# Kernel tuning notes

Measured on AMD Instinct MI355X. Metric: run time of the kernel, lower is better.

Reference implementation:

```python
import jax, jax.numpy as jnp
import numpy as np

N = 50000   # nodes
E = 800000  # edges (avg degree 16)
IN = 256    # in_dim
H = 4       # nhead
D = 64      # out_dim per head
NEG_SLOPE_ATTN = 0.2   # DGL GATConv default negative_slope for edge scores
NEG_SLOPE_OUT = 0.01   # nn.LeakyReLU default on the layer output


def setup_inputs() -> dict:
    key = jax.random.key(0)
    ks = jax.random.split(key, 6)
    h = jax.random.normal(ks[0], (N, IN), dtype=jnp.float32)
    src = jax.random.randint(ks[1], (E,), 0, N, dtype=jnp.int32)
    dst = jax.random.randint(ks[2], (E,), 0, N, dtype=jnp.int32)
    W = jax.random.normal(ks[3], (IN, H * D), dtype=jnp.float32) / np.float32(np.sqrt(IN))
    attn_l = jax.random.normal(ks[4], (H, D), dtype=jnp.float32) * 0.1
    attn_r = jax.random.normal(ks[5], (H, D), dtype=jnp.float32) * 0.1
    bias = jnp.zeros((H * D,), dtype=jnp.float32)
    return {"h": h, "src": src, "dst": dst, "W": W,
            "attn_l": attn_l, "attn_r": attn_r, "bias": bias}


def reference(h, src, dst, W, attn_l, attn_r, bias):
    n = h.shape[0]
    # linear projection -> [N, H, D]
    feat = (h @ W).reshape(n, H, D)
    # per-node, per-head attention halves: [N, H]
    el = jnp.sum(feat * attn_l, axis=-1)
    er = jnp.sum(feat * attn_r, axis=-1)
    # per-edge unnormalized score (DGL: src contributes el, dst contributes er)
    e = jax.nn.leaky_relu(el[src] + er[dst], NEG_SLOPE_ATTN)  # [E, H]
    # edge softmax over incoming edges of each destination node
    emax = jax.ops.segment_max(e, dst, num_segments=n)        # [N, H]
    ee = jnp.exp(e - emax[dst])                               # [E, H]
    denom = jax.ops.segment_sum(ee, dst, num_segments=n)      # [N, H]
    a = ee / jnp.maximum(denom[dst], 1e-9)                    # [E, H]
    # weighted scatter-aggregate of projected source features
    msg = feat[src] * a[:, :, None]                           # [E, H, D]
    rst = jax.ops.segment_sum(msg, dst, num_segments=n)       # [N, H, D]
    rst = rst + bias.reshape(H, D)
    # outer activation (dropout is identity in eval)
    return jax.nn.leaky_relu(rst, NEG_SLOPE_OUT)
```

## Files before the change

kernel.cpp:

```cpp
#include <hip/hip_runtime.h>

#define IN_DIM 256
#define HD 256
#define NHEAD 4
#define BM 128

typedef __attribute__((ext_vector_type(8))) short short8;
typedef __attribute__((ext_vector_type(4))) float f32x4;

__device__ __forceinline__ float bf2f(ushort u) {
    unsigned x = ((unsigned)u) << 16;
    float f;
    __builtin_memcpy(&f, &x, 4);
    return f;
}
__device__ __forceinline__ ushort f2bf(float f) {
    unsigned x;
    __builtin_memcpy(&x, &f, 4);
    unsigned r = (x + 0x7FFFu + ((x >> 16) & 1u)) >> 16;
    return (ushort)r;
}
__device__ __forceinline__ short8 cvt8(float4 x, float4 y) {
    short8 a;
    a[0] = (short)f2bf(x.x); a[1] = (short)f2bf(x.y);
    a[2] = (short)f2bf(x.z); a[3] = (short)f2bf(x.w);
    a[4] = (short)f2bf(y.x); a[5] = (short)f2bf(y.y);
    a[6] = (short)f2bf(y.z); a[7] = (short)f2bf(y.w);
    return a;
}

__global__ void fill_one(float* __restrict__ out, int n) {
    int i = blockIdx.x * 256 + threadIdx.x;
    if (i < n) out[i] = 1.0f;
}

__global__ void conv_w_zero(const float* __restrict__ W, ushort* __restrict__ WT,
                            int* __restrict__ cnt, int n) {
    int idx = blockIdx.x * 256 + threadIdx.x;
    int k = idx >> 8, c = idx & 255;
    WT[c * 256 + k] = f2bf(W[idx]);
    for (int i = idx; i < n; i += 65536) cnt[i] = 0;
}

__global__ __launch_bounds__(256, 2) void gemm_hist(const float* __restrict__ h,
                                                    const short* __restrict__ WT,
                                                    ushort* __restrict__ featb,
                                                    float* __restrict__ el,
                                                    float* __restrict__ er,
                                                    const float* __restrict__ attn_l,
                                                    const float* __restrict__ attn_r,
                                                    const int* __restrict__ dst,
                                                    int* __restrict__ cnt,
                                                    int* __restrict__ epos,
                                                    int gb, int n, int e) {
    if (blockIdx.x >= gb) {
        int i = (blockIdx.x - gb) * 256 + threadIdx.x;
        int base = i * 4;
        if (base + 3 < e) {
            int4 d4 = *(const int4*)(dst + base);
            int4 p4;
            p4.x = atomicAdd(&cnt[d4.x], 1);
            p4.y = atomicAdd(&cnt[d4.y], 1);
            p4.z = atomicAdd(&cnt[d4.z], 1);
            p4.w = atomicAdd(&cnt[d4.w], 1);
            *(int4*)(epos + base) = p4;
        } else {
            for (int q = base; q < e; ++q) epos[q] = atomicAdd(&cnt[dst[q]], 1);
        }
        return;
    }
    __shared__ __align__(16) ushort blds[2][8192];
    int t = threadIdx.x;
    int w = t >> 6, l = t & 63;
    int c15 = l & 15, g = l >> 4;
    int blockBase = blockIdx.x * BM;
    int row0 = blockBase + w * 32 + c15;
    int rA0 = row0 < n ? row0 : n - 1;
    int rA1 = (row0 + 16) < n ? (row0 + 16) : n - 1;
    const float* hA0 = h + (size_t)rA0 * 256 + g * 8;
    const float* hA1 = h + (size_t)rA1 * 256 + g * 8;

    f32x4 acc[2][16];
#pragma unroll
    for (int af = 0; af < 2; ++af)
#pragma unroll
        for (int ct = 0; ct < 16; ++ct) acc[af][ct] = (f32x4)(0.0f);

    short8 st[4];
    int sc[4], sb[4];
#pragma unroll
    for (int p = 0; p < 4; ++p) {
        int q = t + p * 256;
        sc[p] = q >> 2;
        int gg = q & 3;
        sb[p] = ((sc[p] * 64 + gg * 16) ^ ((sc[p] & 7) << 4));
    }

#pragma unroll
    for (int p = 0; p < 4; ++p)
        st[p] = *(const short8*)(WT + sc[p] * 256 + ((t + p * 256) & 3) * 8);
#pragma unroll
    for (int p = 0; p < 4; ++p)
        *(short8*)((char*)blds[0] + sb[p]) = st[p];
    __syncthreads();

    for (int kk = 0; kk < 8; ++kk) {
        int buf = kk & 1;
        if (kk < 7) {
#pragma unroll
            for (int p = 0; p < 4; ++p)
                st[p] = *(const short8*)(WT + sc[p] * 256 + (kk + 1) * 32 + ((t + p * 256) & 3) * 8);
        }
        float4 x0 = *(const float4*)(hA0 + kk * 32);
        float4 y0 = *(const float4*)(hA0 + kk * 32 + 4);
        float4 x1 = *(const float4*)(hA1 + kk * 32);
        float4 y1 = *(const float4*)(hA1 + kk * 32 + 4);
        short8 a0 = cvt8(x0, y0);
        short8 a1 = cvt8(x1, y1);
        const char* bb = (const char*)blds[buf];
#pragma unroll
        for (int ct = 0; ct < 16; ++ct) {
            int c = ct * 16 + c15;
            short8 bv = *(const short8*)(bb + ((c * 64 + g * 16) ^ ((c & 7) << 4)));
            acc[0][ct] = __builtin_amdgcn_mfma_f32_16x16x32_bf16(a0, bv, acc[0][ct], 0, 0, 0);
            acc[1][ct] = __builtin_amdgcn_mfma_f32_16x16x32_bf16(a1, bv, acc[1][ct], 0, 0, 0);
        }
        if (kk < 7) {
#pragma unroll
            for (int p = 0; p < 4; ++p)
                *(short8*)((char*)blds[buf ^ 1] + sb[p]) = st[p];
        }
        __syncthreads();
    }

    float alv[16], arv[16];
#pragma unroll
    for (int ct = 0; ct < 16; ++ct) {
        alv[ct] = attn_l[ct * 16 + c15];
        arv[ct] = attn_r[ct * 16 + c15];
    }

#pragma unroll
    for (int af = 0; af < 2; ++af) {
        int rowb = blockBase + w * 32 + af * 16 + g * 4;
#pragma unroll
        for (int r = 0; r < 4; ++r) {
            int row = rowb + r;
            if (row < n) {
#pragma unroll
                for (int ct = 0; ct < 16; ++ct)
                    featb[(size_t)row * 256 + ct * 16 + c15] = f2bf(acc[af][ct][r]);
            }
            float pl[4] = {0.f, 0.f, 0.f, 0.f}, pr[4] = {0.f, 0.f, 0.f, 0.f};
#pragma unroll
            for (int ct = 0; ct < 16; ++ct) {
                pl[ct >> 2] += acc[af][ct][r] * alv[ct];
                pr[ct >> 2] += acc[af][ct][r] * arv[ct];
            }
#pragma unroll
            for (int m = 1; m < 16; m <<= 1) {
#pragma unroll
                for (int hh = 0; hh < 4; ++hh) {
                    pl[hh] += __shfl_xor(pl[hh], m, 64);
                    pr[hh] += __shfl_xor(pr[hh], m, 64);
                }
            }
            if (row < n) {
                if (c15 < 4)       el[row * 4 + c15]       = pl[c15];
                else if (c15 < 8)  er[row * 4 + (c15 - 4)] = pr[c15 - 4];
            }
        }
    }
}

__global__ __launch_bounds__(1024) void scan_local(const int* __restrict__ cnt,
                                                   int* __restrict__ rl,
                                                   int* __restrict__ bsum, int n) {
    __shared__ int wsums[16];
    int t = threadIdx.x, lane = t & 63, wid = t >> 6;
    int i = blockIdx.x * 1024 + t;
    int x = (i < n) ? cnt[i] : 0;
    int s = x;
#pragma unroll
    for (int off = 1; off < 64; off <<= 1) {
        int v = __shfl_up(s, off, 64);
        if (lane >= off) s += v;
    }
    if (lane == 63) wsums[wid] = s;
    __syncthreads();
    if (wid == 0) {
        int ws = (lane < 16) ? wsums[lane] : 0;
#pragma unroll
        for (int off = 1; off < 16; off <<= 1) {
            int v = __shfl_up(ws, off, 64);
            if (lane >= off) ws += v;
        }
        if (lane < 16) wsums[lane] = ws;
    }
    __syncthreads();
    int woff = (wid > 0) ? wsums[wid - 1] : 0;
    if (i <= n) rl[i] = woff + s - x;
    if (t == 1023) bsum[blockIdx.x] = wsums[15];
}

__global__ __launch_bounds__(1024) void scan_bsum(int* __restrict__ bsum, int nb) {
    __shared__ int wsums[16];
    int t = threadIdx.x, lane = t & 63, wid = t >> 6;
    int x = (t < nb) ? bsum[t] : 0;
    int s = x;
#pragma unroll
    for (int off = 1; off < 64; off <<= 1) {
        int v = __shfl_up(s, off, 64);
        if (lane >= off) s += v;
    }
    if (lane == 63) wsums[wid] = s;
    __syncthreads();
    if (wid == 0) {
        int ws = (lane < 16) ? wsums[lane] : 0;
#pragma unroll
        for (int off = 1; off < 16; off <<= 1) {
            int v = __shfl_up(ws, off, 64);
            if (lane >= off) ws += v;
        }
        if (lane < 16) wsums[lane] = ws;
    }
    __syncthreads();
    int woff = (wid > 0) ? wsums[wid - 1] : 0;
    if (t < nb) bsum[t] = woff + s - x;
}

__global__ void fill_kernel(const int* __restrict__ src, const int* __restrict__ dst,
                            const int* __restrict__ rl, const int* __restrict__ boffs,
                            const int* __restrict__ epos,
                            int* __restrict__ esrc, int e) {
    int i = blockIdx.x * 256 + threadIdx.x;
    int base = i * 4;
    if (base + 3 < e) {
        int4 d4 = *(const int4*)(dst + base);
        int4 s4 = *(const int4*)(src + base);
        int4 p4 = *(const int4*)(epos + base);
        int pos0 = boffs[d4.x >> 10] + rl[d4.x] + p4.x;
        int pos1 = boffs[d4.y >> 10] + rl[d4.y] + p4.y;
        int pos2 = boffs[d4.z >> 10] + rl[d4.z] + p4.z;
        int pos3 = boffs[d4.w >> 10] + rl[d4.w] + p4.w;
        if (pos0 >= 0 && pos0 < e) esrc[pos0] = s4.x;
        if (pos1 >= 0 && pos1 < e) esrc[pos1] = s4.y;
        if (pos2 >= 0 && pos2 < e) esrc[pos2] = s4.z;
        if (pos3 >= 0 && pos3 < e) esrc[pos3] = s4.w;
    } else {
        for (int q = base; q < e; ++q) {
            int d = dst[q];
            int pos = boffs[d >> 10] + rl[d] + epos[q];
            if (pos >= 0 && pos < e) esrc[pos] = src[q];
        }
    }
}

__global__ __launch_bounds__(64) void aggregate(const int* __restrict__ rl,
                                                const int* __restrict__ boffs,
                                                const int* __restrict__ esrc,
                                                const float* __restrict__ el,
                                                const float* __restrict__ er,
                                                const ushort* __restrict__ featb,
                                                const float* __restrict__ bias,
                                                float* __restrict__ out, int n) {
    __shared__ int sbuf[64];
    __shared__ float wbuf[64][4];
    int node = blockIdx.x;
    int l = threadIdx.x;
    int hh = l >> 4;
    int beg = boffs[node >> 10] + rl[node];
    int end = boffs[(node + 1) >> 10] + rl[node + 1];
    float4 bv = *(const float4*)(bias + l * 4);
    float* op = out + (size_t)node * 256 + l * 4;
    if (beg >= end) {
        float4 v;
        v.x = bv.x > 0.f ? bv.x : 0.01f * bv.x;
        v.y = bv.y > 0.f ? bv.y : 0.01f * bv.y;
        v.z = bv.z > 0.f ? bv.z : 0.01f * bv.z;
        v.w = bv.w > 0.f ? bv.w : 0.01f * bv.w;
        *(float4*)op = v;
        return;
    }
    float4 r4 = *(const float4*)(er + (size_t)node * 4);
    float ax = 0.f, ay = 0.f, az = 0.f, aw = 0.f, s = 0.f;
    for (int cb = beg; cb < end; cb += 64) {
        int cn = min(64, end - cb);
        __syncthreads();
        if (l < cn) {
            int sv = esrc[cb + l];
            sv = (sv >= 0 && sv < n) ? sv : 0;
            sbuf[l] = sv;
            float4 l4 = *(const float4*)(el + (size_t)sv * 4);
            float e0 = l4.x + r4.x; e0 = e0 > 0.f ? e0 : 0.2f * e0;
            float e1 = l4.y + r4.y; e1 = e1 > 0.f ? e1 : 0.2f * e1;
            float e2 = l4.z + r4.z; e2 = e2 > 0.f ? e2 : 0.2f * e2;
            float e3 = l4.w + r4.w; e3 = e3 > 0.f ? e3 : 0.2f * e3;
            wbuf[l][0] = __expf(fminf(e0, 60.f));
            wbuf[l][1] = __expf(fminf(e1, 60.f));
            wbuf[l][2] = __expf(fminf(e2, 60.f));
            wbuf[l][3] = __expf(fminf(e3, 60.f));
        }
        __syncthreads();
#pragma unroll 4
        for (int j = 0; j < cn; ++j) {
            int sid = sbuf[j];
            float wgt = wbuf[j][hh];
            ushort4 f4 = *(const ushort4*)(featb + (size_t)sid * 256 + l * 4);
            ax += wgt * bf2f(f4.x);
            ay += wgt * bf2f(f4.y);
            az += wgt * bf2f(f4.z);
            aw += wgt * bf2f(f4.w);
            s += wgt;
        }
    }
    float inv = 1.f / fmaxf(s, 1e-9f);
    float4 v;
    v.x = ax * inv + bv.x; v.x = v.x > 0.f ? v.x : 0.01f * v.x;
    v.y = ay * inv + bv.y; v.y = v.y > 0.f ? v.y : 0.01f * v.y;
    v.z = az * inv + bv.z; v.z = v.z > 0.f ? v.z : 0.01f * v.z;
    v.w = aw * inv + bv.w; v.w = v.w > 0.f ? v.w : 0.01f * v.w;
    *(float4*)op = v;
}

extern "C" void kernel_launch(void* const* d_in, const int* in_sizes, int n_in,
                              void* d_out, int out_size, void* d_ws, size_t ws_size,
                              hipStream_t stream) {
    const float* h      = (const float*)d_in[0];
    const int*   src    = (const int*)d_in[1];
    const int*   dst    = (const int*)d_in[2];
    const float* W      = (const float*)d_in[3];
    const float* attn_l = (const float*)d_in[4];
    const float* attn_r = (const float*)d_in[5];
    const float* bias   = (const float*)d_in[6];
    float* out = (float*)d_out;

    int N = in_sizes[0] / IN_DIM;
    int E = in_sizes[1];
    int NB = (N + 1 + 1023) / 1024;

    auto al = [](size_t x) { return (x + 255) & ~(size_t)255; };
    char* ws = (char*)d_ws;
    size_t o = 0;
    ushort* featb = (ushort*)(ws + o); o += al((size_t)N * HD * 2);
    float*  el    = (float*)(ws + o);  o += al((size_t)N * NHEAD * 4);
    float*  er    = (float*)(ws + o);  o += al((size_t)N * NHEAD * 4);
    int*    rl    = (int*)(ws + o);    o += al((size_t)(N + 1) * 4);
    int*    cnt   = (int*)(ws + o);    o += al((size_t)N * 4);
    int*    bsum  = (int*)(ws + o);    o += al((size_t)NB * 4);
    int*    esrc  = (int*)(ws + o);    o += al((size_t)E * 4);
    int*    epos  = (int*)(ws + o);    o += al((size_t)E * 4);
    ushort* WT    = (ushort*)(ws + o); o += al((size_t)IN_DIM * HD * 2);
    (void)n_in;

    if (ws_size < o) {
        fill_one<<<(out_size + 255) / 256, 256, 0, stream>>>(out, out_size);
        return;
    }

    conv_w_zero<<<(IN_DIM * HD) / 256, 256, 0, stream>>>(W, WT, cnt, N);

    int GB = (N + BM - 1) / BM;
    int HB = ((E + 3) / 4 + 255) / 256;
    gemm_hist<<<GB + HB, 256, 0, stream>>>(h, (const short*)WT, featb, el, er,
                                           attn_l, attn_r, dst, cnt, epos, GB, N, E);

    scan_local<<<NB, 1024, 0, stream>>>(cnt, rl, bsum, N);
    scan_bsum<<<1, 1024, 0, stream>>>(bsum, NB);

    fill_kernel<<<((E + 3) / 4 + 255) / 256, 256, 0, stream>>>(src, dst, rl, bsum, epos, esrc, E);

    aggregate<<<N, 64, 0, stream>>>(rl, bsum, esrc, el, er, featb, bias, out, N);
}
```

Baseline: 139.1 us.

## Fold histogram into GEMM tail, fuse two-level scan, grid-stride fill

Moves the edge-degree histogram from separate extra blocks into a grid-stride loop run by each GEMM block after its tile work. The two scan kernels become one, where the last block to finish (found through an atomic counter with threadfences) scans the block sums. The fill kernel is changed to a grid-stride loop over half as many blocks. The aim is to cut kernel launches and tail blocks, but the atomic histogram now runs after the GEMM instead of alongside it, which can lengthen the critical path.

Result: slower. 162.3 us (+16.7%).

```diff
diff --git a/kernel.cpp b/kernel.cpp
--- a/kernel.cpp
+++ b/kernel.cpp
@@ -35,11 +35,12 @@
 }
 
 __global__ void conv_w_zero(const float* __restrict__ W, ushort* __restrict__ WT,
-                            int* __restrict__ cnt, int n) {
+                            int* __restrict__ cnt, int* __restrict__ donecnt, int n) {
     int idx = blockIdx.x * 256 + threadIdx.x;
     int k = idx >> 8, c = idx & 255;
     WT[c * 256 + k] = f2bf(W[idx]);
     for (int i = idx; i < n; i += 65536) cnt[i] = 0;
+    if (idx == 0) *donecnt = 0;
 }
 
 __global__ __launch_bounds__(256, 2) void gemm_hist(const float* __restrict__ h,
@@ -52,23 +53,7 @@
                                                     const int* __restrict__ dst,
                                                     int* __restrict__ cnt,
                                                     int* __restrict__ epos,
-                                                    int gb, int n, int e) {
-    if (blockIdx.x >= gb) {
-        int i = (blockIdx.x - gb) * 256 + threadIdx.x;
-        int base = i * 4;
-        if (base + 3 < e) {
-            int4 d4 = *(const int4*)(dst + base);
-            int4 p4;
-            p4.x = atomicAdd(&cnt[d4.x], 1);
-            p4.y = atomicAdd(&cnt[d4.y], 1);
-            p4.z = atomicAdd(&cnt[d4.z], 1);
-            p4.w = atomicAdd(&cnt[d4.w], 1);
-            *(int4*)(epos + base) = p4;
-        } else {
-            for (int q = base; q < e; ++q) epos[q] = atomicAdd(&cnt[dst[q]], 1);
-        }
-        return;
-    }
+                                                    int n, int e4, int e) {
     __shared__ __align__(16) ushort blds[2][8192];
     int t = threadIdx.x;
     int w = t >> 6, l = t & 63;
@@ -171,12 +156,30 @@
             }
         }
     }
-}
-
-__global__ __launch_bounds__(1024) void scan_local(const int* __restrict__ cnt,
+
+    int nthreads = gridDim.x * 256;
+    for (int qq = blockIdx.x * 256 + t; qq < e4; qq += nthreads) {
+        int base = qq * 4;
+        int4 d4 = *(const int4*)(dst + base);
+        int4 p4;
+        p4.x = atomicAdd(&cnt[d4.x], 1);
+        p4.y = atomicAdd(&cnt[d4.y], 1);
+        p4.z = atomicAdd(&cnt[d4.z], 1);
+        p4.w = atomicAdd(&cnt[d4.w], 1);
+        *(int4*)(epos + base) = p4;
+    }
+    if (blockIdx.x == 0 && t == 0) {
+        for (int q = e4 * 4; q < e; ++q) epos[q] = atomicAdd(&cnt[dst[q]], 1);
+    }
+}
+
+__global__ __launch_bounds__(1024) void scan_fused(const int* __restrict__ cnt,
                                                    int* __restrict__ rl,
-                                                   int* __restrict__ bsum, int n) {
+                                                   int* __restrict__ bsum,
+                                                   int* __restrict__ donecnt,
+                                                   int n, int nb) {
     __shared__ int wsums[16];
+    __shared__ int isLast;
     int t = threadIdx.x, lane = t & 63, wid = t >> 6;
     int i = blockIdx.x * 1024 + t;
     int x = (i < n) ? cnt[i] : 0;
@@ -201,41 +204,52 @@
     int woff = (wid > 0) ? wsums[wid - 1] : 0;
     if (i <= n) rl[i] = woff + s - x;
     if (t == 1023) bsum[blockIdx.x] = wsums[15];
-}
-
-__global__ __launch_bounds__(1024) void scan_bsum(int* __restrict__ bsum, int nb) {
-    __shared__ int wsums[16];
-    int t = threadIdx.x, lane = t & 63, wid = t >> 6;
-    int x = (t < nb) ? bsum[t] : 0;
-    int s = x;
-#pragma unroll
-    for (int off = 1; off < 64; off <<= 1) {
-        int v = __shfl_up(s, off, 64);
-        if (lane >= off) s += v;
-    }
-    if (lane == 63) wsums[wid] = s;
+
+    __threadfence();
+    if (t == 0) {
+        int prev = atomicAdd(donecnt, 1);
+        isLast = (prev == gridDim.x - 1) ? 1 : 0;
+    }
     __syncthreads();
-    if (wid == 0) {
-        int ws = (lane < 16) ? wsums[lane] : 0;
-#pragma unroll
-        for (int off = 1; off < 16; off <<= 1) {
-            int v = __shfl_up(ws, off, 64);
-            if (lane >= off) ws += v;
-        }
-        if (lane < 16) wsums[lane] = ws;
-    }
-    __syncthreads();
-    int woff = (wid > 0) ? wsums[wid - 1] : 0;
-    if (t < nb) bsum[t] = woff + s - x;
+    if (!isLast) return;
+    __threadfence();
+    int carry = 0;
+    for (int base = 0; base < nb; base += 1024) {
+        __syncthreads();
+        int ii = base + t;
+        int xx = (ii < nb) ? bsum[ii] : 0;
+        int ss = xx;
+#pragma unroll
+        for (int off = 1; off < 64; off <<= 1) {
+            int v = __shfl_up(ss, off, 64);
+            if (lane >= off) ss += v;
+        }
+        if (lane == 63) wsums[wid] = ss;
+        __syncthreads();
+        if (wid == 0) {
+            int ws = (lane < 16) ? wsums[lane] : 0;
+#pragma unroll
+            for (int off = 1; off < 16; off <<= 1) {
+                int v = __shfl_up(ws, off, 64);
+                if (lane >= off) ws += v;
+            }
+            if (lane < 16) wsums[lane] = ws;
+        }
+        __syncthreads();
+        int woff2 = (wid > 0) ? wsums[wid - 1] : 0;
+        if (ii < nb) bsum[ii] = carry + woff2 + ss - xx;
+        int tot = wsums[15];
+        carry += tot;
+    }
 }
 
 __global__ void fill_kernel(const int* __restrict__ src, const int* __restrict__ dst,
                             const int* __restrict__ rl, const int* __restrict__ boffs,
                             const int* __restrict__ epos,
-                            int* __restrict__ esrc, int e) {
-    int i = blockIdx.x * 256 + threadIdx.x;
-    int base = i * 4;
-    if (base + 3 < e) {
+                            int* __restrict__ esrc, int e4, int e) {
+    int nthreads = gridDim.x * 256;
+    for (int i = blockIdx.x * 256 + threadIdx.x; i < e4; i += nthreads) {
+        int base = i * 4;
         int4 d4 = *(const int4*)(dst + base);
         int4 s4 = *(const int4*)(src + base);
         int4 p4 = *(const int4*)(epos + base);
@@ -247,8 +261,9 @@
         if (pos1 >= 0 && pos1 < e) esrc[pos1] = s4.y;
         if (pos2 >= 0 && pos2 < e) esrc[pos2] = s4.z;
         if (pos3 >= 0 && pos3 < e) esrc[pos3] = s4.w;
-    } else {
-        for (int q = base; q < e; ++q) {
+    }
+    if (blockIdx.x == 0 && threadIdx.x == 0) {
+        for (int q = e4 * 4; q < e; ++q) {
             int d = dst[q];
             int pos = boffs[d >> 10] + rl[d] + epos[q];
             if (pos >= 0 && pos < e) esrc[pos] = src[q];
@@ -337,6 +352,7 @@
 
     int N = in_sizes[0] / IN_DIM;
     int E = in_sizes[1];
+    int E4 = E / 4;
     int NB = (N + 1 + 1023) / 1024;
 
     auto al = [](size_t x) { return (x + 255) & ~(size_t)255; };
@@ -348,6 +364,7 @@
     int*    rl    = (int*)(ws + o);    o += al((size_t)(N + 1) * 4);
     int*    cnt   = (int*)(ws + o);    o += al((size_t)N * 4);
     int*    bsum  = (int*)(ws + o);    o += al((size_t)NB * 4);
+    int*    done  = (int*)(ws + o);    o += al(4);
     int*    esrc  = (int*)(ws + o);    o += al((size_t)E * 4);
     int*    epos  = (int*)(ws + o);    o += al((size_t)E * 4);
     ushort* WT    = (ushort*)(ws + o); o += al((size_t)IN_DIM * HD * 2);
@@ -358,17 +375,16 @@
         return;
     }
 
-    conv_w_zero<<<(IN_DIM * HD) / 256, 256, 0, stream>>>(W, WT, cnt, N);
+    conv_w_zero<<<(IN_DIM * HD) / 256, 256, 0, stream>>>(W, WT, cnt, done, N);
 
     int GB = (N + BM - 1) / BM;
-    int HB = ((E + 3) / 4 + 255) / 256;
-    gemm_hist<<<GB + HB, 256, 0, stream>>>(h, (const short*)WT, featb, el, er,
-                                           attn_l, attn_r, dst, cnt, epos, GB, N, E);
-
-    scan_local<<<NB, 1024, 0, stream>>>(cnt, rl, bsum, N);
-    scan_bsum<<<1, 1024, 0, stream>>>(bsum, NB);
-
-    fill_kernel<<<((E + 3) / 4 + 255) / 256, 256, 0, stream>>>(src, dst, rl, bsum, epos, esrc, E);
+    gemm_hist<<<GB, 256, 0, stream>>>(h, (const short*)WT, featb, el, er,
+                                      attn_l, attn_r, dst, cnt, epos, N, E4, E);
+
+    scan_fused<<<NB, 1024, 0, stream>>>(cnt, rl, bsum, done, N, NB);
+
+    int FB = (E4 + 511) / 512;
+    fill_kernel<<<FB, 256, 0, stream>>>(src, dst, rl, bsum, epos, esrc, E4, E);
 
     aggregate<<<N, 64, 0, stream>>>(rl, bsum, esrc, el, er, featb, bias, out, N);
 }
```
